# Kernel tuning notes

Hardware: AMD Instinct MI355X
Metric: run time of the kernel (lower is better)

## Reference

```python
import jax, jax.numpy as jnp
import numpy as np

SHARP = 50.0  # softness of the analytic brush edge


def _rasterize(param, dec, ps):
    # param: [N,12], dec: [N] float 0/1 -> fg,[N,3,ps,ps] (color*alpha*dec), alpha [N,3,ps,ps]
    p = jax.nn.sigmoid(param[:, :8])
    x0, y0 = p[:, 0], p[:, 1]
    wd = jnp.maximum(p[:, 2], 1e-2)
    ht = jnp.maximum(p[:, 3], 1e-2)
    theta = p[:, 4] * jnp.pi
    color = p[:, 5:8]
    lin = (jnp.arange(ps, dtype=param.dtype) + 0.5) / ps
    gy, gx = jnp.meshgrid(lin, lin, indexing='ij')            # [ps,ps]
    dx = gx[None] - x0[:, None, None]
    dy = gy[None] - y0[:, None, None]
    ct = jnp.cos(theta)[:, None, None]
    st = jnp.sin(theta)[:, None, None]
    u = dx * ct + dy * st
    v = -dx * st + dy * ct
    alpha = (jax.nn.sigmoid(SHARP * (wd[:, None, None] / 2 - jnp.abs(u)))
             * jax.nn.sigmoid(SHARP * (ht[:, None, None] / 2 - jnp.abs(v))))
    alpha = alpha * dec[:, None, None]                         # masked scatter == multiply
    alpha3 = jnp.broadcast_to(alpha[:, None], (alpha.shape[0], 3, ps, ps))
    fg = color[:, :, None, None] * alpha3                      # foreground*alpha pre-fused
    return fg, alpha3


def reference(param, decision, cur_canvas):
    b, h, w, s, _ = param.shape
    H, W = cur_canvas.shape[-2], cur_canvas.shape[-1]
    ps = 2 * H // h  # patch_size (== 2*W//w)
    dec = decision.astype(cur_canvas.dtype).reshape(-1)
    fg, al = _rasterize(param.reshape(-1, 12), dec, ps)
    fg = fg.reshape(b, h, w, s, 3, ps, ps)
    al = al.reshape(b, h, w, s, 3, ps, ps)
    q = ps // 4
    canvas = jnp.pad(cur_canvas, ((0, 0), (0, 0), (q, q), (q, q)))
    ey, ex = np.arange(0, h, 2), np.arange(0, w, 2)
    oy, ox = np.arange(1, h, 2), np.arange(1, w, 2)

    def blend(cv, rows, cols, off_y, off_x):
        ny, nx = len(rows), len(cols)
        region = cv[:, :, off_y:off_y + ny * ps, off_x:off_x + nx * ps]
        tiles = region.reshape(b, 3, ny, ps, nx, ps).transpose(0, 2, 4, 1, 3, 5)  # [b,ny,nx,3,ps,ps]
        sf = fg[:, rows][:, :, cols]   # [b,ny,nx,s,3,ps,ps]
        sa = al[:, rows][:, :, cols]
        for i in range(s):
            tiles = sf[:, :, :, i] + tiles * (1.0 - sa[:, :, :, i])
        region = tiles.transpose(0, 3, 1, 4, 2, 5).reshape(b, 3, ny * ps, nx * ps)
        return cv.at[:, :, off_y:off_y + ny * ps, off_x:off_x + nx * ps].set(region)

    canvas = blend(canvas, ey, ex, 0, 0)
    canvas = blend(canvas, oy, ox, ps // 2, ps // 2)
    canvas = blend(canvas, oy, ex, ps // 2, 0)
    canvas = blend(canvas, ey, ox, 0, ps // 2)
    return canvas[:, :, q:-q, q:-q]


def setup_inputs() -> dict:
    key = jax.random.key(0)
    k1, k2, k3 = jax.random.split(key, 3)
    b, h, w, s = 1, 64, 64, 5
    H = W = 1024
    param = jax.random.normal(k1, (b, h, w, s, 12), dtype=jnp.float32)
    decision = jax.random.randint(k2, (b, h, w, s), 0, 2, dtype=jnp.int32)
    cur_canvas = jax.random.uniform(k3, (b, 3, H, W), dtype=jnp.float32)
    return {'param': param, 'decision': decision, 'cur_canvas': cur_canvas}
```

## Files before the change

### kernel.cpp

```cpp
#include <hip/hip_runtime.h>

#define PI_F 3.14159265358979323846f

__device__ __forceinline__ float fexp2(float x) {
#if __has_builtin(__builtin_amdgcn_exp2f)
  return __builtin_amdgcn_exp2f(x);
#else
  return __expf(x * 0.69314718056f);
#endif
}
__device__ __forceinline__ float frcp(float x) {
#if __has_builtin(__builtin_amdgcn_rcpf)
  return __builtin_amdgcn_rcpf(x);
#else
  return 1.0f / x;
#endif
}
__device__ __forceinline__ float fsig(float x) {
  return frcp(1.0f + fexp2(-x * 1.44269504089f));
}

constexpr float SL = 50.0f * 1.44269504089f;

__global__ void prep_kernel(const float* __restrict__ param,
                            const int* __restrict__ dec,
                            float* __restrict__ sp, int n) {
  int sid = blockIdx.x * blockDim.x + threadIdx.x;
  if (sid >= n) return;
  const float4* p4 = (const float4*)(param + (size_t)sid * 12);
  float4 a = p4[0];
  float4 b = p4[1];
  float x0 = fsig(a.x), y0 = fsig(a.y);
  float wd = fmaxf(fsig(a.z), 0.01f);
  float ht = fmaxf(fsig(a.w), 0.01f);
  float th = fsig(b.x) * PI_F;
  float c0 = fsig(b.y), c1 = fsig(b.z), c2 = fsig(b.w);
  float ct = __cosf(th), st = __sinf(th);
  float4* o = (float4*)(sp + (size_t)sid * 12);
  o[0] = make_float4(x0, y0, SL * wd * 0.5f, SL * ht * 0.5f);
  o[1] = make_float4(ct, st, c0, c1);
  o[2] = make_float4(c2, (float)dec[sid], 0.0f, 0.0f);
}

__global__ __launch_bounds__(256) void comp_kernel(
    const float* __restrict__ canvas, const float* __restrict__ sp,
    float* __restrict__ out) {
  const int tx = threadIdx.x & 15, ty = threadIdx.x >> 4;
  const int A = blockIdx.y, B = blockIdx.x;
  const int py = A * 16 + ty, px = B * 16 + tx;
  const int Y = py - 8, X = px - 8;
  if ((unsigned)Y >= 1024u || (unsigned)X >= 1024u) return;

  const int re = (A & 1) ? A - 1 : A;
  const int ro = (A & 1) ? A : A - 1;
  const int ce = (B & 1) ? B - 1 : B;
  const int co = (B & 1) ? B : B - 1;
  const bool re_ok = (unsigned)re < 64u;
  const bool ro_ok = (unsigned)ro < 64u;
  const bool ce_ok = (unsigned)ce < 64u;
  const bool co_ok = (unsigned)co < 64u;

  const size_t pix = (size_t)Y * 1024 + X;
  float v0 = canvas[pix];
  float v1 = canvas[pix + 1024 * 1024];
  float v2 = canvas[pix + 2 * 1024 * 1024];

  const float fx = px + 0.5f, fy = py + 0.5f;

  auto do_tile = [&](int r, int c) {
    const float* __restrict__ tp = sp + (size_t)((r * 64 + c) * 5) * 12;
    const float gx = (fx - (float)(c * 16)) * (1.0f / 32.0f);
    const float gy = (fy - (float)(r * 16)) * (1.0f / 32.0f);
#pragma unroll
    for (int i = 0; i < 5; ++i) {
      const float* q = tp + i * 12;
      const float d = q[9];
      if (d == 0.0f) continue;
      const float dx = gx - q[0];
      const float dy = gy - q[1];
      const float ct = q[4], st = q[5];
      const float u = dx * ct + dy * st;
      const float w = dy * ct - dx * st;
      const float e1 = fexp2(fmaf(SL, fabsf(u), -q[2]));
      const float e2 = fexp2(fmaf(SL, fabsf(w), -q[3]));
      const float al = frcp(1.0f + e1) * frcp(1.0f + e2);
      v0 = fmaf(al, q[6] - v0, v0);
      v1 = fmaf(al, q[7] - v1, v1);
      v2 = fmaf(al, q[8] - v2, v2);
    }
  };
  if (re_ok && ce_ok) do_tile(re, ce);
  if (ro_ok && co_ok) do_tile(ro, co);
  if (ro_ok && ce_ok) do_tile(ro, ce);
  if (re_ok && co_ok) do_tile(re, co);

  out[pix] = v0;
  out[pix + 1024 * 1024] = v1;
  out[pix + 2 * 1024 * 1024] = v2;
}

extern "C" void kernel_launch(void* const* d_in, const int* in_sizes, int n_in,
                              void* d_out, int out_size, void* d_ws, size_t ws_size,
                              hipStream_t stream) {
  const float* param  = (const float*)d_in[0];
  const int*   dec    = (const int*)d_in[1];
  const float* canvas = (const float*)d_in[2];
  float* outp = (float*)d_out;
  float* sp   = (float*)d_ws;

  const int n = 64 * 64 * 5;
  prep_kernel<<<(n + 255) / 256, 256, 0, stream>>>(param, dec, sp, n);
  dim3 grid(65, 65, 1);
  comp_kernel<<<grid, 256, 0, stream>>>(canvas, sp, outp);
}
```

Before: 87.66 us.

## Compact active strokes per tile and stage them in LDS for compositing

The prep kernel now runs once per tile and writes only the strokes whose decision is set, packed into a 64-float record with a count. It also folds the tile offset and the 1/32 scale into the stroke centre and rotation terms. The composite kernel loads the four overlapping tile records into shared memory with a barrier, then loops only over active strokes, with fewer per-pixel operations. This removes per-stroke decision branches and redundant global loads. In exchange it adds a __syncthreads, a data-dependent loop count, and serial per-tile work in prep.

```diff
diff --git a/kernel.cpp b/kernel.cpp
--- a/kernel.cpp
+++ b/kernel.cpp
@@ -1,6 +1,7 @@
 #include <hip/hip_runtime.h>
 
 #define PI_F 3.14159265358979323846f
+constexpr float SL = 50.0f * 1.44269504089f;
 
 __device__ __forceinline__ float fexp2(float x) {
 #if __has_builtin(__builtin_amdgcn_exp2f)
@@ -20,79 +21,99 @@
   return frcp(1.0f + fexp2(-x * 1.44269504089f));
 }
 
-constexpr float SL = 50.0f * 1.44269504089f;
-
-__global__ void prep_kernel(const float* __restrict__ param,
-                            const int* __restrict__ dec,
-                            float* __restrict__ sp, int n) {
-  int sid = blockIdx.x * blockDim.x + threadIdx.x;
-  if (sid >= n) return;
-  const float4* p4 = (const float4*)(param + (size_t)sid * 12);
-  float4 a = p4[0];
-  float4 b = p4[1];
-  float x0 = fsig(a.x), y0 = fsig(a.y);
-  float wd = fmaxf(fsig(a.z), 0.01f);
-  float ht = fmaxf(fsig(a.w), 0.01f);
-  float th = fsig(b.x) * PI_F;
-  float c0 = fsig(b.y), c1 = fsig(b.z), c2 = fsig(b.w);
-  float ct = __cosf(th), st = __sinf(th);
-  float4* o = (float4*)(sp + (size_t)sid * 12);
-  o[0] = make_float4(x0, y0, SL * wd * 0.5f, SL * ht * 0.5f);
-  o[1] = make_float4(ct, st, c0, c1);
-  o[2] = make_float4(c2, (float)dec[sid], 0.0f, 0.0f);
+__global__ void prep_tile(const float* __restrict__ param,
+                          const int* __restrict__ dec,
+                          float* __restrict__ sp) {
+  const int tile = blockIdx.x * blockDim.x + threadIdx.x;
+  if (tile >= 64 * 64) return;
+  const int r = tile >> 6, c = tile & 63;
+  const float4* p4 = (const float4*)(param + (size_t)tile * 5 * 12);
+  const int* dp = dec + tile * 5;
+  float* o = sp + (size_t)tile * 64;
+  int cnt = 0;
+#pragma unroll
+  for (int i = 0; i < 5; ++i) {
+    if (dp[i] != 0) {
+      float4 a = p4[i * 3 + 0];
+      float4 b = p4[i * 3 + 1];
+      float x0 = fsig(a.x), y0 = fsig(a.y);
+      float wd = fmaxf(fsig(a.z), 0.01f);
+      float ht = fmaxf(fsig(a.w), 0.01f);
+      float th = fsig(b.x) * PI_F;
+      float ct = __cosf(th), st = __sinf(th);
+      float4* w4 = (float4*)(o + 4 + cnt * 12);
+      w4[0] = make_float4((float)(c * 16) + 32.0f * x0,
+                          (float)(r * 16) + 32.0f * y0,
+                          ct * (SL / 32.0f), st * (SL / 32.0f));
+      w4[1] = make_float4(SL * wd * 0.5f, SL * ht * 0.5f,
+                          fsig(b.y), fsig(b.z));
+      w4[2] = make_float4(fsig(b.w), 0.0f, 0.0f, 0.0f);
+      ++cnt;
+    }
+  }
+  ((int*)o)[0] = cnt;
 }
 
 __global__ __launch_bounds__(256) void comp_kernel(
     const float* __restrict__ canvas, const float* __restrict__ sp,
     float* __restrict__ out) {
-  const int tx = threadIdx.x & 15, ty = threadIdx.x >> 4;
+  __shared__ float4 lds[4][16];
+
   const int A = blockIdx.y, B = blockIdx.x;
-  const int py = A * 16 + ty, px = B * 16 + tx;
-  const int Y = py - 8, X = px - 8;
-  if ((unsigned)Y >= 1024u || (unsigned)X >= 1024u) return;
-
   const int re = (A & 1) ? A - 1 : A;
   const int ro = (A & 1) ? A : A - 1;
   const int ce = (B & 1) ? B - 1 : B;
   const int co = (B & 1) ? B : B - 1;
-  const bool re_ok = (unsigned)re < 64u;
-  const bool ro_ok = (unsigned)ro < 64u;
-  const bool ce_ok = (unsigned)ce < 64u;
-  const bool co_ok = (unsigned)co < 64u;
+  int tids[4];
+  tids[0] = ((unsigned)re < 64u && (unsigned)ce < 64u) ? re * 64 + ce : -1;
+  tids[1] = ((unsigned)ro < 64u && (unsigned)co < 64u) ? ro * 64 + co : -1;
+  tids[2] = ((unsigned)ro < 64u && (unsigned)ce < 64u) ? ro * 64 + ce : -1;
+  tids[3] = ((unsigned)re < 64u && (unsigned)co < 64u) ? re * 64 + co : -1;
+
+  const int t = threadIdx.x;
+  if (t < 64) {
+    const int k = t >> 4, j = t & 15;
+    const int tid = tids[k];
+    if (tid >= 0)
+      lds[k][j] = ((const float4*)(sp + (size_t)tid * 64))[j];
+    else if (j == 0)
+      lds[k][0] = make_float4(0.0f, 0.0f, 0.0f, 0.0f);
+  }
+  __syncthreads();
+
+  const int tx = t & 15, ty = t >> 4;
+  const int py = A * 16 + ty, px = B * 16 + tx;
+  const int Y = py - 8, X = px - 8;
+  const bool active = ((unsigned)Y < 1024u) & ((unsigned)X < 1024u);
+  if (!active) return;
 
   const size_t pix = (size_t)Y * 1024 + X;
   float v0 = canvas[pix];
   float v1 = canvas[pix + 1024 * 1024];
   float v2 = canvas[pix + 2 * 1024 * 1024];
 
-  const float fx = px + 0.5f, fy = py + 0.5f;
+  const float fx = (float)px + 0.5f, fy = (float)py + 0.5f;
 
-  auto do_tile = [&](int r, int c) {
-    const float* __restrict__ tp = sp + (size_t)((r * 64 + c) * 5) * 12;
-    const float gx = (fx - (float)(c * 16)) * (1.0f / 32.0f);
-    const float gy = (fy - (float)(r * 16)) * (1.0f / 32.0f);
 #pragma unroll
-    for (int i = 0; i < 5; ++i) {
-      const float* q = tp + i * 12;
-      const float d = q[9];
-      if (d == 0.0f) continue;
-      const float dx = gx - q[0];
-      const float dy = gy - q[1];
-      const float ct = q[4], st = q[5];
-      const float u = dx * ct + dy * st;
-      const float w = dy * ct - dx * st;
-      const float e1 = fexp2(fmaf(SL, fabsf(u), -q[2]));
-      const float e2 = fexp2(fmaf(SL, fabsf(w), -q[3]));
+  for (int k = 0; k < 4; ++k) {
+    const float* base = (const float*)&lds[k][0];
+    const int cnt = __float_as_int(base[0]);
+    const float* rec = base + 4;
+    for (int i = 0; i < cnt; ++i) {
+      const float* q = rec + i * 12;
+      const float dxp = fx - q[0];
+      const float dyp = fy - q[1];
+      const float ctp = q[2], stp = q[3];
+      const float u = dxp * ctp + dyp * stp;
+      const float w = dyp * ctp - dxp * stp;
+      const float e1 = fexp2(fabsf(u) - q[4]);
+      const float e2 = fexp2(fabsf(w) - q[5]);
       const float al = frcp(1.0f + e1) * frcp(1.0f + e2);
       v0 = fmaf(al, q[6] - v0, v0);
       v1 = fmaf(al, q[7] - v1, v1);
       v2 = fmaf(al, q[8] - v2, v2);
     }
-  };
-  if (re_ok && ce_ok) do_tile(re, ce);
-  if (ro_ok && co_ok) do_tile(ro, co);
-  if (ro_ok && ce_ok) do_tile(ro, ce);
-  if (re_ok && co_ok) do_tile(re, co);
+  }
 
   out[pix] = v0;
   out[pix + 1024 * 1024] = v1;
@@ -108,8 +129,7 @@
   float* outp = (float*)d_out;
   float* sp   = (float*)d_ws;
 
-  const int n = 64 * 64 * 5;
-  prep_kernel<<<(n + 255) / 256, 256, 0, stream>>>(param, dec, sp, n);
+  prep_tile<<<(4096 + 255) / 256, 256, 0, stream>>>(param, dec, sp);
   dim3 grid(65, 65, 1);
   comp_kernel<<<grid, 256, 0, stream>>>(canvas, sp, outp);
 }
```

Result: faster. 84.20 us (-4.0%).

## Fuse stroke preprocessing into compositing kernel with LDS-compacted live strokes

Applied to the files above, without the earlier changes.

Removes the separate prep kernel. Each 64-thread block now computes sigmoid and trig parameters for its up to 20 overlapping strokes, compacts the live ones into LDS with a ballot and popcount, and has each thread composite a row of 4 pixels using float4 loads and stores. Rotation is applied incrementally across the 4 pixels and the two sigmoids share a single reciprocal. Each stroke's parameters are recomputed by the roughly four blocks that overlap it, in exchange for dropping a launch, the workspace round trip and the per-stroke decision branches.

```diff
diff --git a/kernel.cpp b/kernel.cpp
--- a/kernel.cpp
+++ b/kernel.cpp
@@ -1,6 +1,7 @@
 #include <hip/hip_runtime.h>
 
 #define PI_F 3.14159265358979323846f
+constexpr float SL = 50.0f * 1.44269504089f;
 
 __device__ __forceinline__ float fexp2(float x) {
 #if __has_builtin(__builtin_amdgcn_exp2f)
@@ -20,83 +21,100 @@
   return frcp(1.0f + fexp2(-x * 1.44269504089f));
 }
 
-constexpr float SL = 50.0f * 1.44269504089f;
+__global__ __launch_bounds__(64) void render_kernel(
+    const float* __restrict__ param, const int* __restrict__ dec,
+    const float* __restrict__ canvas, float* __restrict__ out) {
+  __shared__ float4 lds4[20 * 3];
 
-__global__ void prep_kernel(const float* __restrict__ param,
-                            const int* __restrict__ dec,
-                            float* __restrict__ sp, int n) {
-  int sid = blockIdx.x * blockDim.x + threadIdx.x;
-  if (sid >= n) return;
-  const float4* p4 = (const float4*)(param + (size_t)sid * 12);
-  float4 a = p4[0];
-  float4 b = p4[1];
-  float x0 = fsig(a.x), y0 = fsig(a.y);
-  float wd = fmaxf(fsig(a.z), 0.01f);
-  float ht = fmaxf(fsig(a.w), 0.01f);
-  float th = fsig(b.x) * PI_F;
-  float c0 = fsig(b.y), c1 = fsig(b.z), c2 = fsig(b.w);
-  float ct = __cosf(th), st = __sinf(th);
-  float4* o = (float4*)(sp + (size_t)sid * 12);
-  o[0] = make_float4(x0, y0, SL * wd * 0.5f, SL * ht * 0.5f);
-  o[1] = make_float4(ct, st, c0, c1);
-  o[2] = make_float4(c2, (float)dec[sid], 0.0f, 0.0f);
-}
-
-__global__ __launch_bounds__(256) void comp_kernel(
-    const float* __restrict__ canvas, const float* __restrict__ sp,
-    float* __restrict__ out) {
-  const int tx = threadIdx.x & 15, ty = threadIdx.x >> 4;
   const int A = blockIdx.y, B = blockIdx.x;
-  const int py = A * 16 + ty, px = B * 16 + tx;
-  const int Y = py - 8, X = px - 8;
-  if ((unsigned)Y >= 1024u || (unsigned)X >= 1024u) return;
-
   const int re = (A & 1) ? A - 1 : A;
   const int ro = (A & 1) ? A : A - 1;
   const int ce = (B & 1) ? B - 1 : B;
   const int co = (B & 1) ? B : B - 1;
-  const bool re_ok = (unsigned)re < 64u;
-  const bool ro_ok = (unsigned)ro < 64u;
-  const bool ce_ok = (unsigned)ce < 64u;
-  const bool co_ok = (unsigned)co < 64u;
 
-  const size_t pix = (size_t)Y * 1024 + X;
-  float v0 = canvas[pix];
-  float v1 = canvas[pix + 1024 * 1024];
-  float v2 = canvas[pix + 2 * 1024 * 1024];
+  const int j = threadIdx.x;
 
-  const float fx = px + 0.5f, fy = py + 0.5f;
+  bool live = false;
+  float4 w0q, w1q, w2q;
+  if (j < 20) {
+    const int k = j / 5;
+    const int i = j - k * 5;
+    const int rr = (k == 0 || k == 3) ? re : ro;
+    const int cc = (k & 1) ? co : ce;
+    if ((unsigned)rr < 64u && (unsigned)cc < 64u) {
+      const int tid = rr * 64 + cc;
+      const int sid = tid * 5 + i;
+      if (dec[sid] != 0) {
+        const float4* p4 = (const float4*)(param + (size_t)sid * 12);
+        float4 a = p4[0];
+        float4 b = p4[1];
+        float x0 = fsig(a.x), y0 = fsig(a.y);
+        float wd = fmaxf(fsig(a.z), 0.01f);
+        float ht = fmaxf(fsig(a.w), 0.01f);
+        float th = fsig(b.x) * PI_F;
+        float ct = __cosf(th), st = __sinf(th);
+        w0q = make_float4((float)(cc * 16) + 32.0f * x0,
+                          (float)(rr * 16) + 32.0f * y0,
+                          ct * (SL / 32.0f), st * (SL / 32.0f));
+        w1q = make_float4(SL * wd * 0.5f, SL * ht * 0.5f,
+                          fsig(b.y), fsig(b.z));
+        w2q = make_float4(fsig(b.w), 0.0f, 0.0f, 0.0f);
+        live = true;
+      }
+    }
+  }
+  const unsigned long long mask = __ballot(live);
+  const int total = __popcll(mask);
+  if (live) {
+    const int off = __popcll(mask & ((1ull << j) - 1));
+    lds4[off * 3 + 0] = w0q;
+    lds4[off * 3 + 1] = w1q;
+    lds4[off * 3 + 2] = w2q;
+  }
+  __syncthreads();
 
-  auto do_tile = [&](int r, int c) {
-    const float* __restrict__ tp = sp + (size_t)((r * 64 + c) * 5) * 12;
-    const float gx = (fx - (float)(c * 16)) * (1.0f / 32.0f);
-    const float gy = (fy - (float)(r * 16)) * (1.0f / 32.0f);
+  const int cg = j & 3;
+  const int row = j >> 2;
+  const int Xb = B * 16 - 8 + cg * 4;
+  const int Yr = A * 16 - 8 + row;
+  const bool valid = ((unsigned)Xb < 1024u) & ((unsigned)Yr < 1024u);
+  if (!valid) return;
+
+  const size_t pix = (size_t)Yr * 1024 + Xb;
+  float4 v0 = *(const float4*)(canvas + pix);
+  float4 v1 = *(const float4*)(canvas + pix + 1024 * 1024);
+  float4 v2 = *(const float4*)(canvas + pix + 2 * 1024 * 1024);
+
+  const float fx0 = (float)(B * 16 + cg * 4) + 0.5f;
+  const float fy  = (float)(A * 16 + row) + 0.5f;
+
+  for (int s = 0; s < total; ++s) {
+    const float4 qa = lds4[s * 3 + 0];
+    const float4 qb = lds4[s * 3 + 1];
+    const float4 qc = lds4[s * 3 + 2];
+    const float dx0 = fx0 - qa.x;
+    const float dy  = fy - qa.y;
+    float u = dx0 * qa.z + dy * qa.w;
+    float w = dy * qa.z - dx0 * qa.w;
+    float* pv0 = &v0.x;
+    float* pv1 = &v1.x;
+    float* pv2 = &v2.x;
 #pragma unroll
-    for (int i = 0; i < 5; ++i) {
-      const float* q = tp + i * 12;
-      const float d = q[9];
-      if (d == 0.0f) continue;
-      const float dx = gx - q[0];
-      const float dy = gy - q[1];
-      const float ct = q[4], st = q[5];
-      const float u = dx * ct + dy * st;
-      const float w = dy * ct - dx * st;
-      const float e1 = fexp2(fmaf(SL, fabsf(u), -q[2]));
-      const float e2 = fexp2(fmaf(SL, fabsf(w), -q[3]));
-      const float al = frcp(1.0f + e1) * frcp(1.0f + e2);
-      v0 = fmaf(al, q[6] - v0, v0);
-      v1 = fmaf(al, q[7] - v1, v1);
-      v2 = fmaf(al, q[8] - v2, v2);
+    for (int m = 0; m < 4; ++m) {
+      const float e1 = fexp2(fabsf(u) - qb.x);
+      const float e2 = fexp2(fabsf(w) - qb.y);
+      const float al = frcp((1.0f + e1) * (1.0f + e2));
+      pv0[m] = fmaf(al, qb.z - pv0[m], pv0[m]);
+      pv1[m] = fmaf(al, qb.w - pv1[m], pv1[m]);
+      pv2[m] = fmaf(al, qc.x - pv2[m], pv2[m]);
+      u += qa.z;
+      w -= qa.w;
     }
-  };
-  if (re_ok && ce_ok) do_tile(re, ce);
-  if (ro_ok && co_ok) do_tile(ro, co);
-  if (ro_ok && ce_ok) do_tile(ro, ce);
-  if (re_ok && co_ok) do_tile(re, co);
+  }
 
-  out[pix] = v0;
-  out[pix + 1024 * 1024] = v1;
-  out[pix + 2 * 1024 * 1024] = v2;
+  *(float4*)(out + pix) = v0;
+  *(float4*)(out + pix + 1024 * 1024) = v1;
+  *(float4*)(out + pix + 2 * 1024 * 1024) = v2;
 }
 
 extern "C" void kernel_launch(void* const* d_in, const int* in_sizes, int n_in,
@@ -106,10 +124,8 @@
   const int*   dec    = (const int*)d_in[1];
   const float* canvas = (const float*)d_in[2];
   float* outp = (float*)d_out;
-  float* sp   = (float*)d_ws;
+  (void)d_ws; (void)ws_size;
 
-  const int n = 64 * 64 * 5;
-  prep_kernel<<<(n + 255) / 256, 256, 0, stream>>>(param, dec, sp, n);
   dim3 grid(65, 65, 1);
-  comp_kernel<<<grid, 256, 0, stream>>>(canvas, sp, outp);
+  render_kernel<<<grid, 64, 0, stream>>>(param, dec, canvas, outp);
 }
```

New measurement: 79.39 us. 9.4% less time.
